# Performance work log

Hardware: AMD Instinct MI355X
Metric: run time of the kernel (lower is better)

The kernel has to match this reference:

```python
import jax, jax.numpy as jnp
import numpy as np

B, T, C = 4, 2048, 1024
H, D = 16, 64          # n_head, head_dim; H*D == C
FFN = 4096
EPS = 1e-6


def rmsnorm(x, w):
    rms = jnp.sqrt(jnp.mean(x * x, axis=-1, keepdims=True) + EPS)
    return x / rms * w


def l2norm(x):
    n = jnp.sqrt(jnp.sum(x * x, axis=-1, keepdims=True))
    return x / jnp.maximum(n, 1e-12)


def setup_inputs() -> dict:
    key = jax.random.key(0)
    ks = jax.random.split(key, 16)
    s = 0.02
    inp = {
        'x': jax.random.normal(ks[0], (B, T, C), jnp.float32),
        'cos': jax.random.uniform(ks[1], (T, D // 2), jnp.float32),
        'sin': jax.random.uniform(ks[2], (T, D // 2), jnp.float32),
        'norm1_w': jnp.ones((C,), jnp.float32),
        'norm2_w': jnp.ones((C,), jnp.float32),
        'q_w': jax.random.normal(ks[3], (C, C), jnp.float32) * s,
        'k_w': jax.random.normal(ks[4], (C, C), jnp.float32) * s,
        'v_w': jax.random.normal(ks[5], (C, C), jnp.float32) * s,
        'beta_w': jax.random.normal(ks[6], (H, C), jnp.float32) * s,
        'beta_b': jnp.zeros((H,), jnp.float32),
        'gate_w': jax.random.normal(ks[7], (C, C), jnp.float32) * s,
        'o_w': jax.random.normal(ks[8], (C, C), jnp.float32) * s,
        'ffn_gate_w': jax.random.normal(ks[9], (FFN, C), jnp.float32) * s,
        'ffn_up_w': jax.random.normal(ks[10], (FFN, C), jnp.float32) * s,
        'ffn_down_w': jax.random.normal(ks[11], (C, FFN), jnp.float32) * s,
    }
    return inp


def gated_delta_net(xn, q_w, k_w, v_w, beta_w, beta_b, gate_w, o_w):
    # projections -> (B, T, H, D)
    q = (xn @ q_w.T).reshape(B, T, H, D)
    k = (xn @ k_w.T).reshape(B, T, H, D)
    v = (xn @ v_w.T).reshape(B, T, H, D)
    beta = jax.nn.sigmoid(xn @ beta_w.T + beta_b)   # (B, T, H)
    gate = jax.nn.sigmoid(xn @ gate_w.T)            # (B, T, C)
    q = l2norm(q)
    k = l2norm(k)

    # time-major for scan: (T, B, H, D)
    qs = jnp.moveaxis(q, 1, 0)
    ks = jnp.moveaxis(k, 1, 0)
    vs = jnp.moveaxis(v, 1, 0)
    bs = jnp.moveaxis(beta, 1, 0)                   # (T, B, H)

    def step(M, inp):
        q_t, k_t, v_t, b_t = inp
        o_t = jnp.einsum('bhdc,bhc->bhd', M, q_t)
        dv = v_t - jnp.einsum('bhdc,bhc->bhd', M, k_t)
        M = M + b_t[:, :, None, None] * jnp.einsum('bhd,bhc->bhdc', dv, k_t)
        return M, o_t

    M0 = jnp.zeros((B, H, D, D), xn.dtype)
    _, os = jax.lax.scan(step, M0, (qs, ks, vs, bs))  # os: (T, B, H, D)
    o = jnp.moveaxis(os, 0, 1).reshape(B, T, C)
    return (gate * o) @ o_w.T


def swiglu(xn, gate_w, up_w, down_w):
    return (jax.nn.silu(xn @ gate_w.T) * (xn @ up_w.T)) @ down_w.T


def reference(x, cos, sin, norm1_w, norm2_w, q_w, k_w, v_w, beta_w, beta_b,
              gate_w, o_w, ffn_gate_w, ffn_up_w, ffn_down_w):
    # layer_idx=0 -> GatedDeltaNet branch (cos/sin unused, as in torch module)
    x = x + gated_delta_net(rmsnorm(x, norm1_w), q_w, k_w, v_w,
                            beta_w, beta_b, gate_w, o_w)
    x = x + swiglu(rmsnorm(x, norm2_w), ffn_gate_w, ffn_up_w, ffn_down_w)
    return x
```

## Files before the change

kernel.cpp:

```cpp
#include <hip/hip_runtime.h>
#include <stdint.h>

typedef unsigned short u16;
typedef unsigned int   u32;
typedef unsigned long long u64;

typedef __bf16 bf16x8 __attribute__((ext_vector_type(8)));
typedef u16    u16x8  __attribute__((ext_vector_type(8)));
typedef u16    u16x4  __attribute__((ext_vector_type(4)));
typedef float  f32x4  __attribute__((ext_vector_type(4)));

#define BQ 4
#define TT 2048
#define CC 1024
#define HH 16
#define DD 64
#define FF 4096
#define BT 8192
#define NCH 32
#define LCH 64
#define LS 72
#define SE 140
#define FS 132

__device__ __forceinline__ float b2f(u16 v) {
  u32 u = ((u32)v) << 16;
  return __builtin_bit_cast(float, u);
}
__device__ __forceinline__ u16 f2b(float f) {
  u32 u = __builtin_bit_cast(u32, f);
  u32 r = (u + 0x7fffu + ((u >> 16) & 1u)) >> 16;
  return (u16)r;
}
__device__ __forceinline__ bf16x8 ld8(const u16* p) {
  return __builtin_bit_cast(bf16x8, *(const u16x8*)p);
}
__device__ __forceinline__ float sigmoidf_(float x) {
  return 1.0f / (1.0f + __expf(-x));
}

#define MFMA16(a, b, c) __builtin_amdgcn_mfma_f32_16x16x32_bf16(a, b, c, 0, 0, 0)

__device__ __forceinline__ void stage16(const u16* g, u16* lds_base) {
  __builtin_amdgcn_global_load_lds(
      (const __attribute__((address_space(1))) u32*)(uintptr_t)g,
      (__attribute__((address_space(3))) u32*)lds_base, 16, 0, 0);
}

struct Cvt { const float* src; u16* dst; u32 n; u32 pad; };
struct CvtArgs { Cvt d[12]; };

__global__ __launch_bounds__(256) void convert_k(CvtArgs a)
{
  const Cvt c = a.d[blockIdx.y];
  u64 i = ((u64)blockIdx.x * 256 + threadIdx.x) * 8;
  if (i >= c.n) return;
  f32x4 v0 = *(const f32x4*)(c.src + i);
  f32x4 v1 = *(const f32x4*)(c.src + i + 4);
  u16x8 o;
#pragma unroll
  for (int e = 0; e < 4; ++e) { o[e] = f2b(v0[e]); o[e + 4] = f2b(v1[e]); }
  *(u16x8*)(c.dst + i) = o;
}

template <int MODE>
__global__ __launch_bounds__(256) void gemm_bt(
    const u16* __restrict__ A, const u16* __restrict__ Bw,
    void* __restrict__ Cv, const void* __restrict__ res,
    int M, int N, int K)
{
  __shared__ __align__(16) u16 smem[128 * SE];
  const int tid  = threadIdx.x;
  const int lane = tid & 63;
  const int wave = tid >> 6;
  const int bm = blockIdx.x, bn = blockIdx.y;
  const int rw = lane >> 2;
  const int kq = (lane & 3) * 8;
  const int lo = lane & 15;
  const int quad = lane >> 4;
  const int wm = wave & 1, wn = wave >> 1;

  const u16* Ag = A  + (u64)(bm * 128 + wave * 16 + rw) * K + kq;
  const u16* Bg = Bw + (u64)(bn * 128 + wave * 16 + rw) * K + kq;
  u16* const Ab[2] = { smem + wave * 512, smem + 4096 + wave * 512 };
  u16* const Bb[2] = { smem + 8192 + wave * 512, smem + 12288 + wave * 512 };

  f32x4 acc[4][4] = {};
  const int niter = K >> 5;

  stage16(Ag, Ab[0]);
  stage16(Ag + (u64)64 * K, Ab[0] + 2048);
  stage16(Bg, Bb[0]);
  stage16(Bg + (u64)64 * K, Bb[0] + 2048);

  int cur = 0;
  for (int it = 0; it < niter; ++it) {
    __syncthreads();
    if (it + 1 < niter) {
      int kn = (it + 1) << 5;
      stage16(Ag + kn, Ab[cur ^ 1]);
      stage16(Ag + (u64)64 * K + kn, Ab[cur ^ 1] + 2048);
      stage16(Bg + kn, Bb[cur ^ 1]);
      stage16(Bg + (u64)64 * K + kn, Bb[cur ^ 1] + 2048);
    }
    const u16* Ac = smem + cur * 4096;
    const u16* Bc = smem + 8192 + cur * 4096;
    bf16x8 af[4], bq[4];
#pragma unroll
    for (int i = 0; i < 4; ++i)
      af[i] = ld8(Ac + (wm * 64 + i * 16 + lo) * 32 + quad * 8);
#pragma unroll
    for (int j = 0; j < 4; ++j)
      bq[j] = ld8(Bc + (wn * 64 + j * 16 + lo) * 32 + quad * 8);
#pragma unroll
    for (int i = 0; i < 4; ++i)
#pragma unroll
      for (int j = 0; j < 4; ++j)
        acc[i][j] = MFMA16(af[i], bq[j], acc[i][j]);
    cur ^= 1;
  }

  __syncthreads();
  if (MODE == 2) {
    float* Fsm = (float*)smem;
    float* C32 = (float*)Cv;
    const u16* R16 = (const u16*)res;
#pragma unroll
    for (int hh = 0; hh < 2; ++hh) {
      if (wm == hh) {
#pragma unroll
        for (int i = 0; i < 4; ++i)
#pragma unroll
          for (int j = 0; j < 4; ++j)
#pragma unroll
            for (int r = 0; r < 4; ++r)
              Fsm[(i * 16 + quad * 4 + r) * FS + wn * 64 + j * 16 + lo] =
                  acc[i][j][r];
      }
      __syncthreads();
      const int r2 = tid >> 5, c2 = (tid & 31) * 4;
#pragma unroll
      for (int w = 0; w < 8; ++w) {
        int rl = r2 + w * 8;
        f32x4 v = *(const f32x4*)(Fsm + rl * FS + c2);
        u64 off = (u64)(bm * 128 + hh * 64 + rl) * N + bn * 128 + c2;
        u16x4 rr = *(const u16x4*)(R16 + off);
        f32x4 o;
#pragma unroll
        for (int e = 0; e < 4; ++e) o[e] = v[e] + b2f(rr[e]);
        *(f32x4*)(C32 + off) = o;
      }
      __syncthreads();
    }
    return;
  }

#pragma unroll
  for (int i = 0; i < 4; ++i)
#pragma unroll
    for (int j = 0; j < 4; ++j)
#pragma unroll
      for (int r = 0; r < 4; ++r)
        smem[(wm * 64 + i * 16 + quad * 4 + r) * SE + wn * 64 + j * 16 + lo] =
            f2b(acc[i][j][r]);
  __syncthreads();

  u16* C16 = (u16*)Cv;
  const float* R32 = (const float*)res;
  const int orow = tid >> 4, ocol = (tid & 15) * 8;
#pragma unroll
  for (int w = 0; w < 8; ++w) {
    int rl = orow + w * 16;
    u16x8 v = *(const u16x8*)(smem + rl * SE + ocol);
    u64 off = (u64)(bm * 128 + rl) * N + bn * 128 + ocol;
    f32x4 r0 = *(const f32x4*)(R32 + off);
    f32x4 r1 = *(const f32x4*)(R32 + off + 4);
    u16x8 o;
#pragma unroll
    for (int e = 0; e < 4; ++e) {
      o[e]     = f2b(b2f(v[e])     + r0[e]);
      o[e + 4] = f2b(b2f(v[e + 4]) + r1[e]);
    }
    *(u16x8*)(C16 + off) = o;
  }
}

template <int MODE, int SPLIT>
__global__ __launch_bounds__(256, 2) void gemm_bt2(
    const u16* __restrict__ A, const u16* __restrict__ Bw,
    u16* __restrict__ C, const u16* __restrict__ res,
    int M, int N, int K)
{
  __shared__ __align__(16) u16 smem[24576];
  const int tid  = threadIdx.x;
  const int lane = tid & 63;
  const int wave = tid >> 6;
  const int bm = blockIdx.x, bn = blockIdx.y;
  const int rw = lane >> 2;
  const int kq = (lane & 3) * 8;
  const int lo = lane & 15;
  const int quad = lane >> 4;
  const int wm = wave & 1, wn = wave >> 1;

  const u16* Ag = A  + (u64)(bm * 256 + wave * 16 + rw) * K + kq;
  const u16* Bg = Bw + (u64)(bn * 128 + wave * 16 + rw) * K + kq;
  u16* const Ab[2] = { smem + wave * 512, smem + 8192 + wave * 512 };
  u16* const Bb[2] = { smem + 16384 + wave * 512, smem + 20480 + wave * 512 };

  f32x4 acc[8][4] = {};
  const int niter = K >> 5;

#pragma unroll
  for (int r = 0; r < 4; ++r) stage16(Ag + (u64)(64 * r) * K, Ab[0] + r * 2048);
#pragma unroll
  for (int r = 0; r < 2; ++r) stage16(Bg + (u64)(64 * r) * K, Bb[0] + r * 2048);

  int cur = 0;
  for (int it = 0; it < niter; ++it) {
    __syncthreads();
    if (it + 1 < niter) {
      int kn = (it + 1) << 5;
#pragma unroll
      for (int r = 0; r < 4; ++r)
        stage16(Ag + (u64)(64 * r) * K + kn, Ab[cur ^ 1] + r * 2048);
#pragma unroll
      for (int r = 0; r < 2; ++r)
        stage16(Bg + (u64)(64 * r) * K + kn, Bb[cur ^ 1] + r * 2048);
    }
    const u16* Ac = smem + cur * 8192;
    const u16* Bc = smem + 16384 + cur * 4096;
    bf16x8 af[8], bq[4];
#pragma unroll
    for (int i = 0; i < 8; ++i)
      af[i] = ld8(Ac + (wm * 128 + i * 16 + lo) * 32 + quad * 8);
#pragma unroll
    for (int j = 0; j < 4; ++j)
      bq[j] = ld8(Bc + (wn * 64 + j * 16 + lo) * 32 + quad * 8);
#pragma unroll
    for (int i = 0; i < 8; ++i)
#pragma unroll
      for (int j = 0; j < 4; ++j)
        acc[i][j] = MFMA16(af[i], bq[j], acc[i][j]);
    cur ^= 1;
  }

  __syncthreads();
  const int orow = tid >> 4, ocol = (tid & 15) * 8;
#pragma unroll
  for (int hh = 0; hh < 2; ++hh) {
    if (wm == hh) {
#pragma unroll
      for (int i = 0; i < 8; ++i)
#pragma unroll
        for (int j = 0; j < 4; ++j)
#pragma unroll
          for (int r = 0; r < 4; ++r)
            smem[(i * 16 + quad * 4 + r) * SE + wn * 64 + j * 16 + lo] =
                f2b(acc[i][j][r]);
    }
    __syncthreads();
#pragma unroll
    for (int w = 0; w < 8; ++w) {
      int rl = orow + w * 16;
      int row = bm * 256 + hh * 128 + rl;
      u16x8 v = *(const u16x8*)(smem + rl * SE + ocol);
      if (SPLIT) {
        int proj = bn >> 3;
        int colp = (bn & 7) * 128 + ocol;
        *(u16x8*)(C + (u64)proj * BT * CC + (u64)row * CC + colp) = v;
      } else {
        u64 off = (u64)row * N + bn * 128 + ocol;
        if (MODE == 3) {
          u16x8 g = *(const u16x8*)(res + off);
          u16x8 o;
#pragma unroll
          for (int e = 0; e < 8; ++e) {
            float gg = b2f(g[e]);
            o[e] = f2b(gg * sigmoidf_(gg) * b2f(v[e]));
          }
          *(u16x8*)(C + off) = o;
        } else {
          *(u16x8*)(C + off) = v;
        }
      }
    }
    __syncthreads();
  }
}

template <int IN32>
__global__ __launch_bounds__(256) void rmsnorm_k(
    const void* __restrict__ xv, const u16* __restrict__ w, u16* __restrict__ out)
{
  __shared__ float red[4];
  const int row = blockIdx.x, tid = threadIdx.x;
  float v0, v1, v2, v3;
  if (IN32) {
    f32x4 raw = *(const f32x4*)((const float*)xv + (u64)row * CC + tid * 4);
    v0 = raw[0]; v1 = raw[1]; v2 = raw[2]; v3 = raw[3];
  } else {
    u16x4 raw = *(const u16x4*)((const u16*)xv + (u64)row * CC + tid * 4);
    v0 = b2f(raw[0]); v1 = b2f(raw[1]); v2 = b2f(raw[2]); v3 = b2f(raw[3]);
  }
  float s = v0 * v0 + v1 * v1 + v2 * v2 + v3 * v3;
#pragma unroll
  for (int m = 1; m < 64; m <<= 1) s += __shfl_xor(s, m, 64);
  if ((tid & 63) == 0) red[tid >> 6] = s;
  __syncthreads();
  float tot = red[0] + red[1] + red[2] + red[3];
  float r = rsqrtf(tot * (1.0f / CC) + 1e-6f);
  const u16* wr = w + tid * 4;
  u16x4 o;
  o[0] = f2b(v0 * r * b2f(wr[0]));
  o[1] = f2b(v1 * r * b2f(wr[1]));
  o[2] = f2b(v2 * r * b2f(wr[2]));
  o[3] = f2b(v3 * r * b2f(wr[3]));
  *(u16x4*)(out + (u64)row * CC + tid * 4) = o;
}

__global__ __launch_bounds__(256) void l2norm_k(u16* __restrict__ q)
{
  const int row = blockIdx.x, tid = threadIdx.x;
  const int hh = tid >> 4, ss = tid & 15;
  u16* p = q + (u64)row * CC + hh * DD + ss * 4;
  u16x4 raw = *(const u16x4*)p;
  float v0 = b2f(raw[0]), v1 = b2f(raw[1]), v2 = b2f(raw[2]), v3 = b2f(raw[3]);
  float s = v0 * v0 + v1 * v1 + v2 * v2 + v3 * v3;
#pragma unroll
  for (int m = 1; m < 16; m <<= 1) s += __shfl_xor(s, m, 64);
  float sc = 1.0f / fmaxf(sqrtf(s), 1e-12f);
  u16x4 o;
  o[0] = f2b(v0 * sc); o[1] = f2b(v1 * sc);
  o[2] = f2b(v2 * sc); o[3] = f2b(v3 * sc);
  *(u16x4*)p = o;
}

__global__ __launch_bounds__(256) void beta_k(
    const u16* __restrict__ xn, const u16* __restrict__ bw,
    const u16* __restrict__ bb, float* __restrict__ beta)
{
  const int row = blockIdx.x, tid = threadIdx.x;
  const int hh = tid >> 4, ss = tid & 15;
  const u16* xr = xn + (u64)row * CC + ss * 64;
  const u16* wr = bw + (u64)hh * CC + ss * 64;
  float s = 0.f;
#pragma unroll
  for (int j = 0; j < 8; ++j) {
    u16x8 a = *(const u16x8*)(xr + j * 8);
    u16x8 c = *(const u16x8*)(wr + j * 8);
#pragma unroll
    for (int e = 0; e < 8; ++e) s += b2f(a[e]) * b2f(c[e]);
  }
#pragma unroll
  for (int m = 1; m < 16; m <<= 1) s += __shfl_xor(s, m, 64);
  if (ss == 0) beta[(u64)row * HH + hh] = sigmoidf_(s + b2f(bb[hh]));
}

__global__ __launch_bounds__(256) void chunk_pre(
    const u16* __restrict__ qn, const u16* __restrict__ kn,
    const u16* __restrict__ vn, const float* __restrict__ beta,
    u16* __restrict__ wneg, u16* __restrict__ u0m, u16* __restrict__ pm)
{
  __shared__ __align__(16) u16 Qc[64 * LS], Kc[64 * LS], Vc[64 * LS];
  __shared__ float Af[64 * 64];
  __shared__ float bet[64];
  const int tid = threadIdx.x;
  const int lane = tid & 63, wave = tid >> 6;
  const int lo = lane & 15, quad = lane >> 4;
  const int bc = blockIdx.x;
  const int bh = bc >> 5, c = bc & 31;
  const int b = bh >> 4, h = bh & 15;
  const u64 gbase = ((u64)(b * TT + c * LCH) * HH + h) * DD;
  const u64 cb = (u64)bc * 4096;

#pragma unroll
  for (int it = 0; it < 2; ++it) {
    int idx = tid + it * 256;
    int t = idx >> 3, seg = (idx & 7) * 8;
    u64 g = gbase + (u64)t * CC + seg;
    *(u16x8*)(Qc + t * LS + seg) = *(const u16x8*)(qn + g);
    *(u16x8*)(Kc + t * LS + seg) = *(const u16x8*)(kn + g);
    *(u16x8*)(Vc + t * LS + seg) = *(const u16x8*)(vn + g);
  }
  if (tid < 64) bet[tid] = beta[(u64)(b * TT + c * LCH + tid) * HH + h];
  __syncthreads();

  {
    const int wm = wave & 1, wn = wave >> 1;
    f32x4 aa[2][2] = {};
#pragma unroll
    for (int k0 = 0; k0 < 64; k0 += 32) {
      bf16x8 af[2], bq[2];
#pragma unroll
      for (int i = 0; i < 2; ++i) af[i] = ld8(Kc + (wm * 32 + i * 16 + lo) * LS + k0 + quad * 8);
#pragma unroll
      for (int j = 0; j < 2; ++j) bq[j] = ld8(Kc + (wn * 32 + j * 16 + lo) * LS + k0 + quad * 8);
#pragma unroll
      for (int i = 0; i < 2; ++i)
#pragma unroll
        for (int j = 0; j < 2; ++j) aa[i][j] = MFMA16(af[i], bq[j], aa[i][j]);
    }
#pragma unroll
    for (int i = 0; i < 2; ++i)
#pragma unroll
      for (int j = 0; j < 2; ++j)
#pragma unroll
        for (int r = 0; r < 4; ++r) {
          int t = wm * 32 + i * 16 + quad * 4 + r;
          int s = wn * 32 + j * 16 + lo;
          Af[t * 64 + s] = (s < t) ? bet[t] * aa[i][j][r] : 0.0f;
        }
  }
  __syncthreads();

  if (wave < 2) {
    const u16* src = (wave == 0) ? Kc : Vc;
    u16* dst = (wave == 0) ? wneg : u0m;
    const float sgn = (wave == 0) ? -1.0f : 1.0f;
    const int d = lane;
    float hist[64];
#pragma unroll
    for (int t = 0; t < 64; ++t) {
      float a = bet[t] * b2f(src[t * LS + d]);
#pragma unroll
      for (int s = 0; s < t; ++s) a -= Af[t * 64 + s] * hist[s];
      hist[t] = a;
      dst[cb + (u64)t * 64 + d] = f2b(sgn * a);
    }
  } else {
    const int w2 = wave - 2;
    f32x4 ap[2][4] = {};
#pragma unroll
    for (int k0 = 0; k0 < 64; k0 += 32) {
      bf16x8 af[2], bq[4];
#pragma unroll
      for (int i = 0; i < 2; ++i) af[i] = ld8(Qc + (w2 * 32 + i * 16 + lo) * LS + k0 + quad * 8);
#pragma unroll
      for (int j = 0; j < 4; ++j) bq[j] = ld8(Kc + (j * 16 + lo) * LS + k0 + quad * 8);
#pragma unroll
      for (int i = 0; i < 2; ++i)
#pragma unroll
        for (int j = 0; j < 4; ++j) ap[i][j] = MFMA16(af[i], bq[j], ap[i][j]);
    }
#pragma unroll
    for (int i = 0; i < 2; ++i)
#pragma unroll
      for (int j = 0; j < 4; ++j)
#pragma unroll
        for (int r = 0; r < 4; ++r) {
          int t = w2 * 32 + i * 16 + quad * 4 + r;
          int s = j * 16 + lo;
          pm[cb + (u64)t * 64 + s] = f2b((s < t) ? ap[i][j][r] : 0.0f);
        }
  }
}

__global__ __launch_bounds__(256) void chunk_seq(
    const u16* __restrict__ qn, const u16* __restrict__ kn,
    const u16* __restrict__ wneg, const u16* __restrict__ u0m,
    const u16* __restrict__ pm, const u16* __restrict__ gate,
    u16* __restrict__ ob)
{
  __shared__ __align__(16) u16 Qs[64 * LS], KTs[64 * LS], Ws[64 * LS], Ps[64 * LS];
  __shared__ __align__(16) u16 U0q[64 * 16];
  __shared__ __align__(16) u16 Sq[16 * LS], UTq[16 * LS];
  const int tid = threadIdx.x;
  const int lane = tid & 63, wave = tid >> 6;
  const int lo = lane & 15, quad = lane >> 4;
  const int blk = blockIdx.x;
  const int bh = blk >> 2, q = blk & 3;
  const int b = bh >> 4, h = bh & 15;
  f32x4 Sacc = {};

  for (int i = tid; i < 16 * LS; i += 256) Sq[i] = 0;
  __syncthreads();

#pragma unroll 1
  for (int c = 0; c < NCH; ++c) {
    const u64 gbase = ((u64)(b * TT + c * LCH) * HH + h) * DD;
    const u64 cb = (u64)(bh * NCH + c) * 4096;
#pragma unroll
    for (int it = 0; it < 2; ++it) {
      int idx = tid + it * 256;
      int t = idx >> 3, seg = (idx & 7) * 8;
      u64 g = gbase + (u64)t * CC + seg;
      *(u16x8*)(Qs + t * LS + seg) = *(const u16x8*)(qn + g);
      u16x8 kv = *(const u16x8*)(kn + g);
#pragma unroll
      for (int jj = 0; jj < 8; ++jj) KTs[(seg + jj) * LS + t] = kv[jj];
      *(u16x8*)(Ws + t * LS + seg) = *(const u16x8*)(wneg + cb + t * 64 + seg);
      *(u16x8*)(Ps + t * LS + seg) = *(const u16x8*)(pm + cb + t * 64 + seg);
    }
    if (tid < 128) {
      int t = tid >> 1, half = (tid & 1) * 8;
      *(u16x8*)(U0q + t * 16 + half) =
          *(const u16x8*)(u0m + cb + t * 64 + q * 16 + half);
    }
    __syncthreads();

    f32x4 au;
#pragma unroll
    for (int r = 0; r < 4; ++r)
      au[r] = b2f(U0q[(wave * 16 + quad * 4 + r) * 16 + lo]);
#pragma unroll
    for (int k0 = 0; k0 < 64; k0 += 32) {
      bf16x8 af = ld8(Ws + (wave * 16 + lo) * LS + k0 + quad * 8);
      bf16x8 bq = ld8(Sq + lo * LS + k0 + quad * 8);
      au = MFMA16(af, bq, au);
    }
#pragma unroll
    for (int r = 0; r < 4; ++r)
      UTq[lo * LS + wave * 16 + quad * 4 + r] = f2b(au[r]);
    __syncthreads();

    f32x4 ao = {};
#pragma unroll
    for (int k0 = 0; k0 < 64; k0 += 32) {
      bf16x8 af = ld8(Qs + (wave * 16 + lo) * LS + k0 + quad * 8);
      bf16x8 bq = ld8(Sq + lo * LS + k0 + quad * 8);
      ao = MFMA16(af, bq, ao);
    }
#pragma unroll
    for (int k0 = 0; k0 < 64; k0 += 32) {
      bf16x8 af = ld8(Ps + (wave * 16 + lo) * LS + k0 + quad * 8);
      bf16x8 bq = ld8(UTq + lo * LS + k0 + quad * 8);
      ao = MFMA16(af, bq, ao);
    }
#pragma unroll
    for (int r = 0; r < 4; ++r) {
      u64 gidx = gbase + (u64)(wave * 16 + quad * 4 + r) * CC + q * 16 + lo;
      float gg = b2f(gate[gidx]);
      ob[gidx] = f2b(sigmoidf_(gg) * ao[r]);
    }

#pragma unroll
    for (int k0 = 0; k0 < 64; k0 += 32) {
      bf16x8 af = ld8(UTq + lo * LS + k0 + quad * 8);
      bf16x8 bq = ld8(KTs + (wave * 16 + lo) * LS + k0 + quad * 8);
      Sacc = MFMA16(af, bq, Sacc);
    }
    __syncthreads();
#pragma unroll
    for (int r = 0; r < 4; ++r)
      Sq[(quad * 4 + r) * LS + wave * 16 + lo] = f2b(Sacc[r]);
    __syncthreads();
  }
}

extern "C" void kernel_launch(void* const* d_in, const int* in_sizes, int n_in,
                              void* d_out, int out_size, void* d_ws, size_t ws_size,
                              hipStream_t stream)
{
  (void)in_sizes; (void)n_in; (void)out_size; (void)ws_size;
  const float* x32 = (const float*)d_in[0];
  char* ws = (char*)d_ws;
  const u64 SZ = (u64)BT * CC * 2;
  const u64 MB = 1ull << 20;

  u16* xn1  = (u16*)(ws + 0 * SZ);
  u16* qb   = (u16*)(ws + 1 * SZ);
  u16* kb   = (u16*)(ws + 2 * SZ);
  u16* vb   = (u16*)(ws + 3 * SZ);
  u16* grw  = (u16*)(ws + 4 * SZ);
  u16* wneg = (u16*)(ws + 5 * SZ);
  u16* u0m  = (u16*)(ws + 6 * SZ);
  u16* pmm  = (u16*)(ws + 7 * SZ);
  u16* obf  = (u16*)(ws + 8 * SZ);
  u16* x2   = (u16*)(ws + 9 * SZ);
  float* beta = (float*)(ws + 10 * SZ);
  char* CV  = ws + 10 * SZ + MB;
  u16* qwc  = (u16*)(CV + 0 * MB);
  u16* kwc  = (u16*)(CV + 2 * MB);
  u16* vwc  = (u16*)(CV + 4 * MB);
  u16* gwc  = (u16*)(CV + 6 * MB);
  u16* owc  = (u16*)(CV + 8 * MB);
  u16* fgwc = (u16*)(CV + 10 * MB);
  u16* fuwc = (u16*)(CV + 18 * MB);
  u16* fdwc = (u16*)(CV + 26 * MB);
  u16* bwc  = (u16*)(CV + 34 * MB);
  u16* n1c  = (u16*)(CV + 34 * MB + 64 * 1024);
  u16* n2c  = (u16*)(CV + 34 * MB + 80 * 1024);
  u16* bbc  = (u16*)(CV + 34 * MB + 96 * 1024);
  u16* ffg  = (u16*)(ws + 0 * SZ);
  u16* xn2  = obf;

  dim3 blk(256);
  dim3 g1(BT / 128, CC / 128);
  dim3 g2(BT / 256, FF / 128);

  CvtArgs ca;
  ca.d[0]  = { (const float*)d_in[5],  qwc,  (u32)(CC * CC), 0 };
  ca.d[1]  = { (const float*)d_in[6],  kwc,  (u32)(CC * CC), 0 };
  ca.d[2]  = { (const float*)d_in[7],  vwc,  (u32)(CC * CC), 0 };
  ca.d[3]  = { (const float*)d_in[10], gwc,  (u32)(CC * CC), 0 };
  ca.d[4]  = { (const float*)d_in[11], owc,  (u32)(CC * CC), 0 };
  ca.d[5]  = { (const float*)d_in[12], fgwc, (u32)(FF * CC), 0 };
  ca.d[6]  = { (const float*)d_in[13], fuwc, (u32)(FF * CC), 0 };
  ca.d[7]  = { (const float*)d_in[14], fdwc, (u32)(CC * FF), 0 };
  ca.d[8]  = { (const float*)d_in[8],  bwc,  (u32)(HH * CC), 0 };
  ca.d[9]  = { (const float*)d_in[3],  n1c,  (u32)CC, 0 };
  ca.d[10] = { (const float*)d_in[4],  n2c,  (u32)CC, 0 };
  ca.d[11] = { (const float*)d_in[9],  bbc,  (u32)HH, 0 };
  convert_k<<<dim3(2048, 12), blk, 0, stream>>>(ca);

  rmsnorm_k<1><<<BT, blk, 0, stream>>>(x32, n1c, xn1);
  gemm_bt2<0, 1><<<g2, blk, 0, stream>>>(xn1, qwc, qb, nullptr, BT, FF, CC);
  beta_k<<<BT, blk, 0, stream>>>(xn1, bwc, bbc, beta);
  l2norm_k<<<BT, blk, 0, stream>>>(qb);
  l2norm_k<<<BT, blk, 0, stream>>>(kb);
  chunk_pre<<<BQ * HH * NCH, blk, 0, stream>>>(qb, kb, vb, beta, wneg, u0m, pmm);
  chunk_seq<<<BQ * HH * 4, blk, 0, stream>>>(qb, kb, wneg, u0m, pmm, grw, obf);
  gemm_bt<1><<<g1, blk, 0, stream>>>(obf, owc, x2, x32, BT, CC, CC);
  rmsnorm_k<0><<<BT, blk, 0, stream>>>(x2, n2c, xn2);
  gemm_bt2<0, 0><<<g2, blk, 0, stream>>>(xn2, fgwc, ffg, nullptr, BT, FF, CC);
  gemm_bt2<3, 0><<<g2, blk, 0, stream>>>(xn2, fuwc, ffg, ffg, BT, FF, CC);
  gemm_bt<2><<<g1, blk, 0, stream>>>(ffg, fdwc, d_out, x2, BT, CC, FF);
}
```

Baseline: 734.1 us.

## Triple-buffer LDS staging in GEMM kernels with explicit vmcnt waits

Result: faster. 711.6 us (-3.1%).

```diff
diff --git a/kernel.cpp b/kernel.cpp
--- a/kernel.cpp
+++ b/kernel.cpp
@@ -47,6 +47,8 @@
       (__attribute__((address_space(3))) u32*)lds_base, 16, 0, 0);
 }
 
+#define BAR_VM(N) asm volatile("s_waitcnt vmcnt(" #N ")\n\ts_barrier" ::: "memory")
+
 struct Cvt { const float* src; u16* dst; u32 n; u32 pad; };
 struct CvtArgs { Cvt d[12]; };
 
@@ -64,47 +66,47 @@
 }
 
 template <int MODE>
-__global__ __launch_bounds__(256) void gemm_bt(
+__global__ __launch_bounds__(256, 3) void gemm_bt(
     const u16* __restrict__ A, const u16* __restrict__ Bw,
     void* __restrict__ Cv, const void* __restrict__ res,
     int M, int N, int K)
 {
-  __shared__ __align__(16) u16 smem[128 * SE];
+  __shared__ __align__(16) u16 smem[24576];
   const int tid  = threadIdx.x;
   const int lane = tid & 63;
   const int wave = tid >> 6;
   const int bm = blockIdx.x, bn = blockIdx.y;
-  const int rw = lane >> 2;
-  const int kq = (lane & 3) * 8;
   const int lo = lane & 15;
   const int quad = lane >> 4;
   const int wm = wave & 1, wn = wave >> 1;
 
+  const int rw = lane >> 2;
+  const int kq = (lane & 3) * 8;
   const u16* Ag = A  + (u64)(bm * 128 + wave * 16 + rw) * K + kq;
   const u16* Bg = Bw + (u64)(bn * 128 + wave * 16 + rw) * K + kq;
-  u16* const Ab[2] = { smem + wave * 512, smem + 4096 + wave * 512 };
-  u16* const Bb[2] = { smem + 8192 + wave * 512, smem + 12288 + wave * 512 };
 
   f32x4 acc[4][4] = {};
   const int niter = K >> 5;
 
-  stage16(Ag, Ab[0]);
-  stage16(Ag + (u64)64 * K, Ab[0] + 2048);
-  stage16(Bg, Bb[0]);
-  stage16(Bg + (u64)64 * K, Bb[0] + 2048);
-
-  int cur = 0;
+  auto stage = [&](int t, int s) {
+    int kk = t << 5;
+    u16* base = smem + s * 8192;
+    stage16(Ag + kk,                 base + wave * 512);
+    stage16(Ag + (u64)64 * K + kk,   base + 2048 + wave * 512);
+    stage16(Bg + kk,                 base + 4096 + wave * 512);
+    stage16(Bg + (u64)64 * K + kk,   base + 4096 + 2048 + wave * 512);
+  };
+
+  stage(0, 0);
+  stage(1, 1);
+
+  int sc = 0, sp = 2;
   for (int it = 0; it < niter; ++it) {
-    __syncthreads();
-    if (it + 1 < niter) {
-      int kn = (it + 1) << 5;
-      stage16(Ag + kn, Ab[cur ^ 1]);
-      stage16(Ag + (u64)64 * K + kn, Ab[cur ^ 1] + 2048);
-      stage16(Bg + kn, Bb[cur ^ 1]);
-      stage16(Bg + (u64)64 * K + kn, Bb[cur ^ 1] + 2048);
-    }
-    const u16* Ac = smem + cur * 4096;
-    const u16* Bc = smem + 8192 + cur * 4096;
+    if (it + 1 < niter) BAR_VM(4);
+    else BAR_VM(0);
+    if (it + 2 < niter) stage(it + 2, sp);
+    const u16* Ac = smem + sc * 8192;
+    const u16* Bc = Ac + 4096;
     bf16x8 af[4], bq[4];
 #pragma unroll
     for (int i = 0; i < 4; ++i)
@@ -117,7 +119,8 @@
 #pragma unroll
       for (int j = 0; j < 4; ++j)
         acc[i][j] = MFMA16(af[i], bq[j], acc[i][j]);
-    cur ^= 1;
+    sc = (sc == 2) ? 0 : sc + 1;
+    sp = (sp == 2) ? 0 : sp + 1;
   }
 
   __syncthreads();
@@ -191,44 +194,44 @@
     u16* __restrict__ C, const u16* __restrict__ res,
     int M, int N, int K)
 {
-  __shared__ __align__(16) u16 smem[24576];
+  __shared__ __align__(16) u16 smem[36864];
   const int tid  = threadIdx.x;
   const int lane = tid & 63;
   const int wave = tid >> 6;
   const int bm = blockIdx.x, bn = blockIdx.y;
-  const int rw = lane >> 2;
-  const int kq = (lane & 3) * 8;
   const int lo = lane & 15;
   const int quad = lane >> 4;
   const int wm = wave & 1, wn = wave >> 1;
 
+  const int rw = lane >> 2;
+  const int kq = (lane & 3) * 8;
   const u16* Ag = A  + (u64)(bm * 256 + wave * 16 + rw) * K + kq;
   const u16* Bg = Bw + (u64)(bn * 128 + wave * 16 + rw) * K + kq;
-  u16* const Ab[2] = { smem + wave * 512, smem + 8192 + wave * 512 };
-  u16* const Bb[2] = { smem + 16384 + wave * 512, smem + 20480 + wave * 512 };
 
   f32x4 acc[8][4] = {};
   const int niter = K >> 5;
 
-#pragma unroll
-  for (int r = 0; r < 4; ++r) stage16(Ag + (u64)(64 * r) * K, Ab[0] + r * 2048);
-#pragma unroll
-  for (int r = 0; r < 2; ++r) stage16(Bg + (u64)(64 * r) * K, Bb[0] + r * 2048);
-
-  int cur = 0;
+  auto stage = [&](int t, int s) {
+    int kk = t << 5;
+    u16* base = smem + s * 12288;
+#pragma unroll
+    for (int r = 0; r < 4; ++r)
+      stage16(Ag + (u64)(64 * r) * K + kk, base + r * 2048 + wave * 512);
+#pragma unroll
+    for (int r = 0; r < 2; ++r)
+      stage16(Bg + (u64)(64 * r) * K + kk, base + 8192 + r * 2048 + wave * 512);
+  };
+
+  stage(0, 0);
+  stage(1, 1);
+
+  int sc = 0, sp = 2;
   for (int it = 0; it < niter; ++it) {
-    __syncthreads();
-    if (it + 1 < niter) {
-      int kn = (it + 1) << 5;
-#pragma unroll
-      for (int r = 0; r < 4; ++r)
-        stage16(Ag + (u64)(64 * r) * K + kn, Ab[cur ^ 1] + r * 2048);
-#pragma unroll
-      for (int r = 0; r < 2; ++r)
-        stage16(Bg + (u64)(64 * r) * K + kn, Bb[cur ^ 1] + r * 2048);
-    }
-    const u16* Ac = smem + cur * 8192;
-    const u16* Bc = smem + 16384 + cur * 4096;
+    if (it + 1 < niter) BAR_VM(6);
+    else BAR_VM(0);
+    if (it + 2 < niter) stage(it + 2, sp);
+    const u16* Ac = smem + sc * 12288;
+    const u16* Bc = Ac + 8192;
     bf16x8 af[8], bq[4];
 #pragma unroll
     for (int i = 0; i < 8; ++i)
@@ -241,7 +244,8 @@
 #pragma unroll
       for (int j = 0; j < 4; ++j)
         acc[i][j] = MFMA16(af[i], bq[j], acc[i][j]);
-    cur ^= 1;
+    sc = (sc == 2) ? 0 : sc + 1;
+    sp = (sp == 2) ? 0 : sp + 1;
   }
 
   __syncthreads();
```
